# Kernel tuning notes

Hardware: AMD Instinct MI355X
Metric: run time of the kernel (lower is better)

The kernel has to match this reference:

```python
import jax, jax.numpy as jnp
import numpy as np

N = 4096          # in_features == out_features, power of two
DEPTH = 12        # log2(N) butterfly stages
TOKENS = 8192     # flattened batch*seq tokens


def setup_inputs() -> dict:
    key = jax.random.key(0)
    kx, kf, kb = jax.random.split(key, 3)
    x = jax.random.normal(kx, (TOKENS, N), dtype=jnp.float32)
    # factors initialized as identity 2x2 blocks + small noise, as in __init__
    eye = jnp.broadcast_to(jnp.eye(2, dtype=jnp.float32), (DEPTH, N // 2, 2, 2))
    factors = eye + 0.01 * jax.random.normal(kf, (DEPTH, N // 2, 2, 2), dtype=jnp.float32)
    bias = 0.01 * jax.random.normal(kb, (N,), dtype=jnp.float32)
    return {"x": x, "factors": factors, "bias": bias}


def _apply_stage(x, factor, stage):
    # Faithful translation of ButterflyLinear._apply_stage
    B, n = x.shape
    block = 1 << (stage + 1)
    half = block >> 1
    m = n // block
    # (B, m, half, 2) -> permute -> (B, m, 2, half)
    staged = x.reshape(B, m, half, 2).transpose(0, 1, 3, 2)
    pairs = staged.reshape(B, n // 2, 2)           # N/2 pairs per token
    t = jnp.einsum('bnc,ncd->bnd', pairs, factor)  # tiny 2x2 block matmuls
    t = t.reshape(B, m, 2, half).transpose(0, 1, 3, 2)
    return t.reshape(B, n)


def reference(x, factors, bias):
    out = x
    for stage in range(factors.shape[0]):  # fixed small DEPTH loop (structural)
        out = _apply_stage(out, factors[stage], stage)
    return out + bias
```

## Files before the change

### kernel.cpp

```cpp
#include <hip/hip_runtime.h>


#define NFEAT   4096
#define DEPTH   12
#define NPAIR   (NFEAT / 2)
#define NGROUPS (NFEAT / 4)
#define GBLK    256
#define TOK_PER_BLK 16
#define TOKENS  8192

__global__ __launch_bounds__(GBLK)
void butterfly_kernel(const float* __restrict__ x,
                      const float* __restrict__ factors,
                      const float* __restrict__ bias,
                      float* __restrict__ out)
{
    const int k    = blockIdx.x * GBLK + threadIdx.x;
    const int tok0 = blockIdx.y * TOK_PER_BLK;

    float4 f[DEPTH][2];
    f[0][0] = *(const float4*)(factors + (size_t)(0 * NPAIR + 2 * k    ) * 4);
    f[0][1] = *(const float4*)(factors + (size_t)(0 * NPAIR + 2 * k + 1) * 4);
#pragma unroll
    for (int s = 1; s < DEPTH; ++s) {
        const int lowmask = (1 << (s - 1)) - 1;
        const int p0 = ((k >> (s - 1)) << s) | (k & lowmask);
        const int p1 = p0 + (1 << (s - 1));
        f[s][0] = *(const float4*)(factors + (size_t)(s * NPAIR + p0) * 4);
        f[s][1] = *(const float4*)(factors + (size_t)(s * NPAIR + p1) * 4);
    }
    const float4 bv = *(const float4*)(bias + 4 * k);

    for (int t = 0; t < TOK_PER_BLK; ++t) {
        const int b = tok0 + t;
        float4 v = *(const float4*)(x + (size_t)b * NFEAT + 4 * k);

        {
            const float n0 = v.x * f[0][0].x + v.y * f[0][0].z;
            const float n1 = v.x * f[0][0].y + v.y * f[0][0].w;
            const float n2 = v.z * f[0][1].x + v.w * f[0][1].z;
            const float n3 = v.z * f[0][1].y + v.w * f[0][1].w;
            v = make_float4(n0, n1, n2, n3);
        }
#pragma unroll
        for (int s = 1; s < DEPTH; ++s) {
            const float n0 = v.x * f[s][0].x + v.z * f[s][0].z;
            const float n2 = v.x * f[s][0].y + v.z * f[s][0].w;
            const float n1 = v.y * f[s][1].x + v.w * f[s][1].z;
            const float n3 = v.y * f[s][1].y + v.w * f[s][1].w;
            v = make_float4(n0, n1, n2, n3);
        }

        v.x += bv.x; v.y += bv.y; v.z += bv.z; v.w += bv.w;
        *(float4*)(out + (size_t)b * NFEAT + 4 * k) = v;
    }
}

extern "C" void kernel_launch(void* const* d_in, const int* in_sizes, int n_in,
                              void* d_out, int out_size, void* d_ws, size_t ws_size,
                              hipStream_t stream) {
    const float* x       = (const float*)d_in[0];
    const float* factors = (const float*)d_in[1];
    const float* bias    = (const float*)d_in[2];
    float* out           = (float*)d_out;

    dim3 grid(NGROUPS / GBLK, TOKENS / TOK_PER_BLK);
    dim3 block(GBLK);
    butterfly_kernel<<<grid, block, 0, stream>>>(x, factors, bias, out);
}
```

Measured before the change: 241.1 us.

## Precompose butterfly stages into per-group 4x4 matrices, apply with nontemporal IO

Adds a small kernel that multiplies the twelve 2x2 butterfly stages, for each 4-element group, into one 4x4 matrix written to workspace. The apply kernel then does a single 4x4 matvec plus bias per token, replacing twelve stages of FMAs, and uses nontemporal loads and stores. Tokens per block drop from 16 to 8. This removes per-token stage arithmetic and the factor registers, at the cost of an extra launch and reliance on the workspace buffer. The kernel is memory-bound, so the arithmetic savings may matter less than the access pattern.

```diff
diff --git a/kernel.cpp b/kernel.cpp
--- a/kernel.cpp
+++ b/kernel.cpp
@@ -5,54 +5,83 @@
 #define DEPTH   12
 #define NPAIR   (NFEAT / 2)
 #define NGROUPS (NFEAT / 4)
+#define TOKENS  8192
 #define GBLK    256
-#define TOK_PER_BLK 16
-#define TOKENS  8192
+#define TOK_PER_BLK 8
 
-__global__ __launch_bounds__(GBLK)
-void butterfly_kernel(const float* __restrict__ x,
-                      const float* __restrict__ factors,
-                      const float* __restrict__ bias,
-                      float* __restrict__ out)
+typedef float fx4 __attribute__((ext_vector_type(4)));
+
+__device__ __forceinline__ float4 stage0_apply(float4 v, float4 a, float4 b) {
+    return make_float4(v.x * a.x + v.y * a.z,
+                       v.x * a.y + v.y * a.w,
+                       v.z * b.x + v.w * b.z,
+                       v.z * b.y + v.w * b.w);
+}
+__device__ __forceinline__ float4 stageS_apply(float4 v, float4 a, float4 b) {
+    return make_float4(v.x * a.x + v.z * a.z,
+                       v.y * b.x + v.w * b.z,
+                       v.x * a.y + v.z * a.w,
+                       v.y * b.y + v.w * b.w);
+}
+
+__global__ __launch_bounds__(256)
+void compose_kernel(const float* __restrict__ factors, float* __restrict__ M)
 {
-    const int k    = blockIdx.x * GBLK + threadIdx.x;
-    const int tok0 = blockIdx.y * TOK_PER_BLK;
+    const int k = blockIdx.x * 256 + threadIdx.x;
 
-    float4 f[DEPTH][2];
-    f[0][0] = *(const float4*)(factors + (size_t)(0 * NPAIR + 2 * k    ) * 4);
-    f[0][1] = *(const float4*)(factors + (size_t)(0 * NPAIR + 2 * k + 1) * 4);
+    float4 c0 = make_float4(1.f, 0.f, 0.f, 0.f);
+    float4 c1 = make_float4(0.f, 1.f, 0.f, 0.f);
+    float4 c2 = make_float4(0.f, 0.f, 1.f, 0.f);
+    float4 c3 = make_float4(0.f, 0.f, 0.f, 1.f);
+
+    {
+        const float4 a = *(const float4*)(factors + (size_t)(2 * k    ) * 4);
+        const float4 b = *(const float4*)(factors + (size_t)(2 * k + 1) * 4);
+        c0 = stage0_apply(c0, a, b);
+        c1 = stage0_apply(c1, a, b);
+        c2 = stage0_apply(c2, a, b);
+        c3 = stage0_apply(c3, a, b);
+    }
 #pragma unroll
     for (int s = 1; s < DEPTH; ++s) {
         const int lowmask = (1 << (s - 1)) - 1;
         const int p0 = ((k >> (s - 1)) << s) | (k & lowmask);
         const int p1 = p0 + (1 << (s - 1));
-        f[s][0] = *(const float4*)(factors + (size_t)(s * NPAIR + p0) * 4);
-        f[s][1] = *(const float4*)(factors + (size_t)(s * NPAIR + p1) * 4);
+        const float4 a = *(const float4*)(factors + (size_t)(s * NPAIR + p0) * 4);
+        const float4 b = *(const float4*)(factors + (size_t)(s * NPAIR + p1) * 4);
+        c0 = stageS_apply(c0, a, b);
+        c1 = stageS_apply(c1, a, b);
+        c2 = stageS_apply(c2, a, b);
+        c3 = stageS_apply(c3, a, b);
     }
+
+    float4* m = (float4*)(M + (size_t)k * 16);
+    m[0] = c0; m[1] = c1; m[2] = c2; m[3] = c3;
+}
+
+__global__ __launch_bounds__(GBLK)
+void apply_kernel(const float* __restrict__ x,
+                  const float* __restrict__ M,
+                  const float* __restrict__ bias,
+                  float* __restrict__ out)
+{
+    const int k    = blockIdx.x * GBLK + threadIdx.x;
+    const int tok0 = blockIdx.y * TOK_PER_BLK;
+
+    const float4* m = (const float4*)(M + (size_t)k * 16);
+    const float4 c0 = m[0], c1 = m[1], c2 = m[2], c3 = m[3];
     const float4 bv = *(const float4*)(bias + 4 * k);
 
+#pragma unroll
     for (int t = 0; t < TOK_PER_BLK; ++t) {
-        const int b = tok0 + t;
-        float4 v = *(const float4*)(x + (size_t)b * NFEAT + 4 * k);
-
-        {
-            const float n0 = v.x * f[0][0].x + v.y * f[0][0].z;
-            const float n1 = v.x * f[0][0].y + v.y * f[0][0].w;
-            const float n2 = v.z * f[0][1].x + v.w * f[0][1].z;
-            const float n3 = v.z * f[0][1].y + v.w * f[0][1].w;
-            v = make_float4(n0, n1, n2, n3);
-        }
-#pragma unroll
-        for (int s = 1; s < DEPTH; ++s) {
-            const float n0 = v.x * f[s][0].x + v.z * f[s][0].z;
-            const float n2 = v.x * f[s][0].y + v.z * f[s][0].w;
-            const float n1 = v.y * f[s][1].x + v.w * f[s][1].z;
-            const float n3 = v.y * f[s][1].y + v.w * f[s][1].w;
-            v = make_float4(n0, n1, n2, n3);
-        }
-
-        v.x += bv.x; v.y += bv.y; v.z += bv.z; v.w += bv.w;
-        *(float4*)(out + (size_t)b * NFEAT + 4 * k) = v;
+        const size_t off = (size_t)(tok0 + t) * NFEAT + 4 * k;
+        const fx4 vv = __builtin_nontemporal_load((const fx4*)(x + off));
+        fx4 r;
+        r.x = bv.x + vv.x * c0.x + vv.y * c1.x + vv.z * c2.x + vv.w * c3.x;
+        r.y = bv.y + vv.x * c0.y + vv.y * c1.y + vv.z * c2.y + vv.w * c3.y;
+        r.z = bv.z + vv.x * c0.z + vv.y * c1.z + vv.z * c2.z + vv.w * c3.z;
+        r.w = bv.w + vv.x * c0.w + vv.y * c1.w + vv.z * c2.w + vv.w * c3.w;
+        __builtin_nontemporal_store(r, (fx4*)(out + off));
     }
 }
 
@@ -63,8 +92,10 @@
     const float* factors = (const float*)d_in[1];
     const float* bias    = (const float*)d_in[2];
     float* out           = (float*)d_out;
+    float* M             = (float*)d_ws;
+
+    compose_kernel<<<dim3(NGROUPS / 256), dim3(256), 0, stream>>>(factors, M);
 
     dim3 grid(NGROUPS / GBLK, TOKENS / TOK_PER_BLK);
-    dim3 block(GBLK);
-    butterfly_kernel<<<grid, block, 0, stream>>>(x, factors, bias, out);
+    apply_kernel<<<grid, dim3(GBLK), 0, stream>>>(x, M, bias, out);
 }
```

Measured after the change: 228.5 us. 1.06x faster.
